# Performance work log

Measured on AMD Instinct MI355X. Metric: run time of the kernel, lower is better.

## Reference

```python
import jax, jax.numpy as jnp
import numpy as np

TOKENS = 8192
IN_FEATURES = 4096
OUT_FEATURES = 4096
ALPHA = 2e-05
BETA = 8.0


def setup_inputs() -> dict:
    key = jax.random.key(0)
    kx, kw = jax.random.split(key)
    # int8 activations and weights, values in [-127, 127]
    x = jax.random.randint(kx, (TOKENS, IN_FEATURES), -127, 128, dtype=jnp.int32).astype(jnp.int8)
    weight = jax.random.randint(kw, (OUT_FEATURES, IN_FEATURES), -127, 128, dtype=jnp.int32).astype(jnp.int8)
    bias = jnp.zeros((OUT_FEATURES,), dtype=jnp.float32)
    a = jnp.float32(ALPHA)  # dequant scale: input_scale * weight_scale
    b = jnp.float32(BETA)   # requant scale: 1 / out_scale
    return {"x": x, "weight": weight, "bias": bias, "a": a, "b": b}


def reference(x, weight, bias, a, b):
    acc = jnp.matmul(x.astype(jnp.int32), weight.T.astype(jnp.int32))
    # fp32 epilogue: dequant scale + bias, exact GeLU, requant by beta
    y = a * acc.astype(jnp.float32) + bias[None, :]
    y = jax.nn.gelu(y, approximate=False)
    # quantize output to int8 (round to nearest even, saturate)
    q = jnp.clip(jnp.rint(y * b), -128.0, 127.0).astype(jnp.int8)
    return q
```

## Files before the change

kernel.cpp:

```cpp
#include <hip/hip_runtime.h>
#include <cstdint>
#include <cstddef>

#define TOKENS 8192
#define INF    4096
#define OUTF   4096

typedef int v4i __attribute__((ext_vector_type(4)));

__global__ __launch_bounds__(256) void pack_i8_kernel(
    const int* __restrict__ xi, const int* __restrict__ wi,
    uint8_t* __restrict__ x8, uint8_t* __restrict__ w8) {
  const int NX = (TOKENS * INF) / 4;
  const int NT = 2048 * 256;
  int tid = blockIdx.x * 256 + threadIdx.x;
#pragma unroll 1
  for (int it = 0; it < 24; ++it) {
    int c = it * NT + tid;
    const int4* src;
    unsigned* dst;
    if (c < NX) {
      src = (const int4*)xi + c;
      dst = (unsigned*)x8 + c;
    } else {
      int c2 = c - NX;
      src = (const int4*)wi + c2;
      dst = (unsigned*)w8 + c2;
    }
    int4 v = *src;
    *dst = (v.x & 255) | ((v.y & 255) << 8) | ((v.z & 255) << 16) |
           (((unsigned)v.w) << 24);
  }
}

__device__ __forceinline__ float gelu_exact(float y) {
  float x = y * 0.70710678118654752f;
  float s = fabsf(x);
  float t = __builtin_amdgcn_rcpf(fmaf(s, 0.3275911f, 1.0f));
  float p = t * fmaf(t, fmaf(t, fmaf(t, fmaf(t, 1.061405429f, -1.453152027f),
                                     1.421413741f), -0.284496736f),
                     0.254829592f);
  float e = __expf(-s * s);
  float er = fmaf(-p, e, 1.0f);
  er = copysignf(er, x);
  return 0.5f * y * (1.0f + er);
}

__global__ __launch_bounds__(512, 2) void gemm_i8_gelu_q_kernel(
    const uint8_t* __restrict__ x8, const uint8_t* __restrict__ w8,
    const float* __restrict__ bias, const float* __restrict__ pa,
    const float* __restrict__ pb, int* __restrict__ out) {
  __shared__ char sm[65536];

  const int tid = threadIdx.x;
  const int l   = tid & 63;
  const int wv  = tid >> 6;
  const int wr  = wv >> 2;
  const int wc  = wv & 3;
  const int lr  = l & 15;
  const int lg  = l >> 4;

  int id = blockIdx.x;
  int wg = (id & 7) * 64 + (id >> 3);
  const int m0 = (wg >> 4) * 256;
  const int n0 = (wg & 15) * 256;

  const float av = pa[0];
  const float bv = pb[0];

  const int srow  = tid >> 3;
  const int sslot = tid & 7;
  const int wslot = ((sslot ^ (srow & 7)) << 4);
  const uint8_t* ga = x8 + (size_t)(m0 + srow) * INF + sslot * 16;
  const uint8_t* gb = w8 + (size_t)(n0 + srow) * INF + sslot * 16;
  const int lds_w = srow * 128 + wslot;

  int aoff[8], boff[4], sb[2];
#pragma unroll
  for (int m = 0; m < 8; ++m) aoff[m] = (wr * 128 + m * 16 + lr) * 128;
#pragma unroll
  for (int n = 0; n < 4; ++n) boff[n] = 32768 + (wc * 64 + n * 16 + lr) * 128;
#pragma unroll
  for (int s = 0; s < 2; ++s) sb[s] = (((s * 4 + lg) ^ (l & 7)) << 4);

  v4i acc[8][4];
#pragma unroll
  for (int m = 0; m < 8; ++m)
#pragma unroll
    for (int n = 0; n < 4; ++n) acc[m][n] = (v4i){0, 0, 0, 0};

  v4i avr[4], bvr[4];
#pragma unroll
  for (int i = 0; i < 4; ++i) {
    avr[i] = *(const v4i*)(ga + (size_t)i * 64 * INF);
    bvr[i] = *(const v4i*)(gb + (size_t)i * 64 * INF);
  }

  const int NKT = INF / 128;
#pragma unroll 1
  for (int kt = 0; kt < NKT; ++kt) {
    asm volatile("" ::: "memory");
    __builtin_amdgcn_s_barrier();
    asm volatile("" ::: "memory");
#pragma unroll
    for (int i = 0; i < 4; ++i) {
      *(v4i*)(sm + i * 8192 + lds_w)         = avr[i];
      *(v4i*)(sm + 32768 + i * 8192 + lds_w) = bvr[i];
    }
    __syncthreads();

    if (kt + 1 < NKT) {
      const uint8_t* ga2 = ga + (size_t)(kt + 1) * 128;
      const uint8_t* gb2 = gb + (size_t)(kt + 1) * 128;
#pragma unroll
      for (int i = 0; i < 4; ++i) {
        avr[i] = *(const v4i*)(ga2 + (size_t)i * 64 * INF);
        bvr[i] = *(const v4i*)(gb2 + (size_t)i * 64 * INF);
      }
    }

#pragma unroll
    for (int s = 0; s < 2; ++s) {
      v4i Af[8], Bf[4];
#pragma unroll
      for (int m = 0; m < 8; ++m) Af[m] = *(const v4i*)(sm + aoff[m] + sb[s]);
#pragma unroll
      for (int n = 0; n < 4; ++n) Bf[n] = *(const v4i*)(sm + boff[n] + sb[s]);
#pragma unroll
      for (int m = 0; m < 8; ++m)
#pragma unroll
        for (int n = 0; n < 4; ++n)
          acc[m][n] = __builtin_amdgcn_mfma_i32_16x16x64_i8(Af[m], Bf[n],
                                                            acc[m][n], 0, 0, 0);
    }
  }

  float bvals[4];
#pragma unroll
  for (int n = 0; n < 4; ++n) bvals[n] = bias[n0 + wc * 64 + n * 16 + lr];

#pragma unroll
  for (int m = 0; m < 8; ++m) {
    int rowb = m0 + wr * 128 + m * 16 + lg * 4;
#pragma unroll
    for (int q = 0; q < 4; ++q) {
      size_t rb = (size_t)(rowb + q) * OUTF;
#pragma unroll
      for (int n = 0; n < 4; ++n) {
        float f = fmaf(av, (float)acc[m][n][q], bvals[n]);
        float g = gelu_exact(f);
        float r = __builtin_rintf(g * bv);
        r = fminf(fmaxf(r, -128.0f), 127.0f);
        out[rb + (size_t)(n0 + wc * 64 + n * 16 + lr)] = (int)r;
      }
    }
  }
}

extern "C" void kernel_launch(void* const* d_in, const int* in_sizes, int n_in,
                              void* d_out, int out_size, void* d_ws,
                              size_t ws_size, hipStream_t stream) {
  const int*   xi   = (const int*)d_in[0];
  const int*   wi   = (const int*)d_in[1];
  const float* bias = (const float*)d_in[2];
  const float* pa   = (const float*)d_in[3];
  const float* pb   = (const float*)d_in[4];
  int*         out  = (int*)d_out;

  uint8_t* x8 = (uint8_t*)d_ws;
  uint8_t* w8 = x8 + (size_t)TOKENS * INF;

  pack_i8_kernel<<<2048, 256, 0, stream>>>(xi, wi, x8, w8);

  dim3 grid((TOKENS / 256) * (OUTF / 256));
  gemm_i8_gelu_q_kernel<<<grid, 512, 0, stream>>>(x8, w8, bias, pa, pb, out);
}
```

Baseline: 417.6 us.

## Use direct global-to-LDS loads with double-buffered LDS and phased MFMA scheduling

Replaces the register-staged global loads and LDS stores with global_load_lds direct-to-LDS transfers into a double-buffered 128KB shared memory region, prefetching two k-tiles ahead. The compute loop is split into four phases separated by barriers, with s_setprio raised around MFMA bursts so waves interleave LDS reads and matrix ops. The intent is to remove VGPR staging and LDS write instructions and to overlap memory traffic with compute. The cost is double the LDS use, which with 512 threads and a 2-block launch bound may limit occupancy to one block per CU, plus extra barriers per tile.

```diff
diff --git a/kernel.cpp b/kernel.cpp
--- a/kernel.cpp
+++ b/kernel.cpp
@@ -46,11 +46,17 @@
   return 0.5f * y * (1.0f + er);
 }
 
+__device__ __forceinline__ void barrier_fenced() {
+  asm volatile("" ::: "memory");
+  __builtin_amdgcn_s_barrier();
+  asm volatile("" ::: "memory");
+}
+
 __global__ __launch_bounds__(512, 2) void gemm_i8_gelu_q_kernel(
     const uint8_t* __restrict__ x8, const uint8_t* __restrict__ w8,
     const float* __restrict__ bias, const float* __restrict__ pa,
     const float* __restrict__ pb, int* __restrict__ out) {
-  __shared__ char sm[65536];
+  __shared__ char sm[131072];
 
   const int tid = threadIdx.x;
   const int l   = tid & 63;
@@ -68,12 +74,11 @@
   const float av = pa[0];
   const float bv = pb[0];
 
-  const int srow  = tid >> 3;
-  const int sslot = tid & 7;
-  const int wslot = ((sslot ^ (srow & 7)) << 4);
-  const uint8_t* ga = x8 + (size_t)(m0 + srow) * INF + sslot * 16;
-  const uint8_t* gb = w8 + (size_t)(n0 + srow) * INF + sslot * 16;
-  const int lds_w = srow * 128 + wslot;
+  const int grow = (wv << 5) + (l >> 3);
+  const int gch  = ((l & 7) ^ ((l >> 3) & 7)) << 4;
+  const uint8_t* gA = x8 + (size_t)(m0 + grow) * INF + gch;
+  const uint8_t* gB = w8 + (size_t)(n0 + grow) * INF + gch;
+  const int ldsw = (wv << 2) * 1024;
 
   int aoff[8], boff[4], sb[2];
 #pragma unroll
@@ -89,50 +94,76 @@
 #pragma unroll
     for (int n = 0; n < 4; ++n) acc[m][n] = (v4i){0, 0, 0, 0};
 
-  v4i avr[4], bvr[4];
-#pragma unroll
-  for (int i = 0; i < 4; ++i) {
-    avr[i] = *(const v4i*)(ga + (size_t)i * 64 * INF);
-    bvr[i] = *(const v4i*)(gb + (size_t)i * 64 * INF);
-  }
+#define BURST(kt, bo)                                                         \
+  {                                                                           \
+    _Pragma("unroll")                                                         \
+    for (int i = 0; i < 4; ++i) {                                             \
+      __builtin_amdgcn_global_load_lds(                                       \
+          (const __attribute__((address_space(1))) unsigned*)(                \
+              gA + (size_t)i * 8 * INF + (size_t)(kt) * 128),                 \
+          (__attribute__((address_space(3))) unsigned*)(sm + (bo) + ldsw +    \
+                                                        i * 1024),            \
+          16, 0, 0);                                                          \
+      __builtin_amdgcn_global_load_lds(                                       \
+          (const __attribute__((address_space(1))) unsigned*)(                \
+              gB + (size_t)i * 8 * INF + (size_t)(kt) * 128),                 \
+          (__attribute__((address_space(3))) unsigned*)(sm + (bo) + 32768 +   \
+                                                        ldsw + i * 1024),     \
+          16, 0, 0);                                                          \
+    }                                                                         \
+  }
+
+#define LDV4(off) (*(const v4i*)(sm + bo + (off)))
+
+#define PHASE(mb, ks, READB)                                                  \
+  {                                                                           \
+    if (READB) {                                                              \
+      _Pragma("unroll")                                                       \
+      for (int n = 0; n < 4; ++n) Bf[n] = LDV4(boff[n] + sb[ks]);             \
+    }                                                                         \
+    v4i A0 = LDV4(aoff[(mb) + 0] + sb[ks]);                                   \
+    v4i A1 = LDV4(aoff[(mb) + 1] + sb[ks]);                                   \
+    v4i A2 = LDV4(aoff[(mb) + 2] + sb[ks]);                                   \
+    v4i A3 = LDV4(aoff[(mb) + 3] + sb[ks]);                                   \
+    barrier_fenced();                                                         \
+    asm volatile("s_waitcnt lgkmcnt(0)" ::: "memory");                        \
+    __builtin_amdgcn_s_setprio(1);                                            \
+    _Pragma("unroll")                                                         \
+    for (int n = 0; n < 4; ++n) {                                             \
+      acc[(mb) + 0][n] = __builtin_amdgcn_mfma_i32_16x16x64_i8(               \
+          A0, Bf[n], acc[(mb) + 0][n], 0, 0, 0);                              \
+      acc[(mb) + 1][n] = __builtin_amdgcn_mfma_i32_16x16x64_i8(               \
+          A1, Bf[n], acc[(mb) + 1][n], 0, 0, 0);                              \
+      acc[(mb) + 2][n] = __builtin_amdgcn_mfma_i32_16x16x64_i8(               \
+          A2, Bf[n], acc[(mb) + 2][n], 0, 0, 0);                              \
+      acc[(mb) + 3][n] = __builtin_amdgcn_mfma_i32_16x16x64_i8(               \
+          A3, Bf[n], acc[(mb) + 3][n], 0, 0, 0);                              \
+    }                                                                         \
+    __builtin_amdgcn_s_setprio(0);                                            \
+    __builtin_amdgcn_s_barrier();                                             \
+    asm volatile("" ::: "memory");                                            \
+  }
+
+  BURST(0, 0);
+  BURST(1, 65536);
 
   const int NKT = INF / 128;
 #pragma unroll 1
   for (int kt = 0; kt < NKT; ++kt) {
-    asm volatile("" ::: "memory");
-    __builtin_amdgcn_s_barrier();
-    asm volatile("" ::: "memory");
-#pragma unroll
-    for (int i = 0; i < 4; ++i) {
-      *(v4i*)(sm + i * 8192 + lds_w)         = avr[i];
-      *(v4i*)(sm + 32768 + i * 8192 + lds_w) = bvr[i];
+    const int bo = (kt & 1) << 16;
+    if (kt < NKT - 1) {
+      asm volatile("s_waitcnt vmcnt(8)" ::: "memory");
+    } else {
+      asm volatile("s_waitcnt vmcnt(0)" ::: "memory");
     }
-    __syncthreads();
-
-    if (kt + 1 < NKT) {
-      const uint8_t* ga2 = ga + (size_t)(kt + 1) * 128;
-      const uint8_t* gb2 = gb + (size_t)(kt + 1) * 128;
-#pragma unroll
-      for (int i = 0; i < 4; ++i) {
-        avr[i] = *(const v4i*)(ga2 + (size_t)i * 64 * INF);
-        bvr[i] = *(const v4i*)(gb2 + (size_t)i * 64 * INF);
-      }
-    }
-
-#pragma unroll
-    for (int s = 0; s < 2; ++s) {
-      v4i Af[8], Bf[4];
-#pragma unroll
-      for (int m = 0; m < 8; ++m) Af[m] = *(const v4i*)(sm + aoff[m] + sb[s]);
-#pragma unroll
-      for (int n = 0; n < 4; ++n) Bf[n] = *(const v4i*)(sm + boff[n] + sb[s]);
-#pragma unroll
-      for (int m = 0; m < 8; ++m)
-#pragma unroll
-        for (int n = 0; n < 4; ++n)
-          acc[m][n] = __builtin_amdgcn_mfma_i32_16x16x64_i8(Af[m], Bf[n],
-                                                            acc[m][n], 0, 0, 0);
-    }
+    barrier_fenced();
+
+    v4i Bf[4];
+    PHASE(0, 0, 1)
+    PHASE(4, 0, 0)
+    PHASE(0, 1, 1)
+    PHASE(4, 1, 0)
+    if (kt + 2 < NKT) BURST(kt + 2, bo);
   }
 
   float bvals[4];
@@ -155,6 +186,9 @@
       }
     }
   }
+#undef BURST
+#undef LDV4
+#undef PHASE
 }
 
 extern "C" void kernel_launch(void* const* d_in, const int* in_sizes, int n_in,
```

After: 425.3 us. No clear change (+1.9%).

## Pipeline GEMM mainloop with direct global-to-LDS loads and 4-stage LDS ring

Applied to the files above, without the earlier changes.

Replaces the register-staged global load plus LDS store with global_load_lds direct copies into a 4-slot LDS ring of 64-byte K halves, issuing loads three stages ahead. The MFMA work is split into quarter blocks interleaved with partial fragment reads, barriers and setprio, to overlap memory and matrix math. The pack kernel also batches four independent loads per iteration to expose memory-level parallelism. LDS use doubles to 128 KB per block, which may limit occupancy to one block per CU, and the hand-counted vmcnt waits add correctness fragility.

```diff
diff --git a/kernel.cpp b/kernel.cpp
--- a/kernel.cpp
+++ b/kernel.cpp
@@ -15,21 +15,23 @@
   const int NT = 2048 * 256;
   int tid = blockIdx.x * 256 + threadIdx.x;
 #pragma unroll 1
-  for (int it = 0; it < 24; ++it) {
-    int c = it * NT + tid;
-    const int4* src;
-    unsigned* dst;
-    if (c < NX) {
-      src = (const int4*)xi + c;
-      dst = (unsigned*)x8 + c;
-    } else {
-      int c2 = c - NX;
-      src = (const int4*)wi + c2;
-      dst = (unsigned*)w8 + c2;
+  for (int g = 0; g < 6; ++g) {
+    int c[4];
+    int4 v[4];
+#pragma unroll
+    for (int j = 0; j < 4; ++j) {
+      c[j] = (g * 4 + j) * NT + tid;
+      const int4* src = (c[j] < NX) ? ((const int4*)xi + c[j])
+                                    : ((const int4*)wi + (c[j] - NX));
+      v[j] = *src;
     }
-    int4 v = *src;
-    *dst = (v.x & 255) | ((v.y & 255) << 8) | ((v.z & 255) << 16) |
-           (((unsigned)v.w) << 24);
+#pragma unroll
+    for (int j = 0; j < 4; ++j) {
+      unsigned* dst = (c[j] < NX) ? ((unsigned*)x8 + c[j])
+                                  : ((unsigned*)w8 + (c[j] - NX));
+      *dst = (v[j].x & 255) | ((v[j].y & 255) << 8) | ((v[j].z & 255) << 16) |
+             (((unsigned)v[j].w) << 24);
+    }
   }
 }
 
@@ -46,11 +48,17 @@
   return 0.5f * y * (1.0f + er);
 }
 
+__device__ __forceinline__ void barrier_fenced() {
+  asm volatile("" ::: "memory");
+  __builtin_amdgcn_s_barrier();
+  asm volatile("" ::: "memory");
+}
+
 __global__ __launch_bounds__(512, 2) void gemm_i8_gelu_q_kernel(
     const uint8_t* __restrict__ x8, const uint8_t* __restrict__ w8,
     const float* __restrict__ bias, const float* __restrict__ pa,
     const float* __restrict__ pb, int* __restrict__ out) {
-  __shared__ char sm[65536];
+  __shared__ char sm[131072];
 
   const int tid = threadIdx.x;
   const int l   = tid & 63;
@@ -68,20 +76,19 @@
   const float av = pa[0];
   const float bv = pb[0];
 
-  const int srow  = tid >> 3;
-  const int sslot = tid & 7;
-  const int wslot = ((sslot ^ (srow & 7)) << 4);
-  const uint8_t* ga = x8 + (size_t)(m0 + srow) * INF + sslot * 16;
-  const uint8_t* gb = w8 + (size_t)(n0 + srow) * INF + sslot * 16;
-  const int lds_w = srow * 128 + wslot;
-
-  int aoff[8], boff[4], sb[2];
-#pragma unroll
-  for (int m = 0; m < 8; ++m) aoff[m] = (wr * 128 + m * 16 + lr) * 128;
-#pragma unroll
-  for (int n = 0; n < 4; ++n) boff[n] = 32768 + (wc * 64 + n * 16 + lr) * 128;
-#pragma unroll
-  for (int s = 0; s < 2; ++s) sb[s] = (((s * 4 + lg) ^ (l & 7)) << 4);
+  const int srow4 = l >> 2;
+  const int schu  = ((l & 3) ^ (srow4 & 3)) << 4;
+  const uint8_t* bA = x8 + (size_t)(m0 + wv * 16 + srow4) * INF + schu;
+  const uint8_t* bB = w8 + (size_t)(n0 + wv * 16 + srow4) * INF + schu;
+  const int dA = wv * 1024;
+
+  int aoff[8], boff[4];
+#pragma unroll
+  for (int m = 0; m < 8; ++m)
+    aoff[m] = (wr * 128 + m * 16 + lr) * 64 + ((lg ^ (lr & 3)) << 4);
+#pragma unroll
+  for (int n = 0; n < 4; ++n)
+    boff[n] = 65536 + (wc * 64 + n * 16 + lr) * 64 + ((lg ^ (lr & 3)) << 4);
 
   v4i acc[8][4];
 #pragma unroll
@@ -89,51 +96,92 @@
 #pragma unroll
     for (int n = 0; n < 4; ++n) acc[m][n] = (v4i){0, 0, 0, 0};
 
-  v4i avr[4], bvr[4];
-#pragma unroll
-  for (int i = 0; i < 4; ++i) {
-    avr[i] = *(const v4i*)(ga + (size_t)i * 64 * INF);
-    bvr[i] = *(const v4i*)(gb + (size_t)i * 64 * INF);
-  }
-
-  const int NKT = INF / 128;
+#define GLL(gsrc, ldst)                                                       \
+  __builtin_amdgcn_global_load_lds(                                           \
+      (const __attribute__((address_space(1))) unsigned*)(gsrc),              \
+      (__attribute__((address_space(3))) unsigned*)(ldst), 16, 0, 0);
+
+#define GLA(H, J) GLL(bA + (size_t)(H) * 64 + (size_t)(J) * 128 * INF,        \
+                      sm + (((H) & 3) << 14) + (J) * 8192 + dA)
+#define GLB(H, J) GLL(bB + (size_t)(H) * 64 + (size_t)(J) * 128 * INF,        \
+                      sm + 65536 + (((H) & 3) << 14) + (J) * 8192 + dA)
+
+#define MM(m, n) acc[m][n] = __builtin_amdgcn_mfma_i32_16x16x64_i8(           \
+                     Af[m], Bf[n], acc[m][n], 0, 0, 0)
+
+#define PRE_MFMA                                                              \
+  barrier_fenced();                                                           \
+  asm volatile("s_waitcnt lgkmcnt(0)" ::: "memory");                          \
+  __builtin_amdgcn_s_setprio(1);
+#define POST_MFMA                                                             \
+  __builtin_amdgcn_s_setprio(0);                                              \
+  barrier_fenced();
+
+#define HALF(H, S, DOSTAGE, NW)                                               \
+  {                                                                           \
+    const char* sb_ = sm + ((S) << 14);                                       \
+    v4i Af[8], Bf[4];                                                         \
+                                        \
+    Af[0] = *(const v4i*)(sb_ + aoff[0]);                                     \
+    Af[1] = *(const v4i*)(sb_ + aoff[1]);                                     \
+    Af[2] = *(const v4i*)(sb_ + aoff[2]);                                     \
+    Af[3] = *(const v4i*)(sb_ + aoff[3]);                                     \
+    Bf[0] = *(const v4i*)(sb_ + boff[0]);                                     \
+    Bf[1] = *(const v4i*)(sb_ + boff[1]);                                     \
+    if (DOSTAGE) { GLA((H) + 3, 0); }                                         \
+    PRE_MFMA                                                                  \
+    MM(0, 0); MM(0, 1); MM(1, 0); MM(1, 1);                                   \
+    MM(2, 0); MM(2, 1); MM(3, 0); MM(3, 1);                                   \
+    POST_MFMA                                                                 \
+                                             \
+    Af[4] = *(const v4i*)(sb_ + aoff[4]);                                     \
+    Af[5] = *(const v4i*)(sb_ + aoff[5]);                                     \
+    Af[6] = *(const v4i*)(sb_ + aoff[6]);                                     \
+    Af[7] = *(const v4i*)(sb_ + aoff[7]);                                     \
+    if (DOSTAGE) { GLA((H) + 3, 1); }                                         \
+    PRE_MFMA                                                                  \
+    MM(4, 0); MM(4, 1); MM(5, 0); MM(5, 1);                                   \
+    MM(6, 0); MM(6, 1); MM(7, 0); MM(7, 1);                                   \
+    POST_MFMA                                                                 \
+                                             \
+    Bf[2] = *(const v4i*)(sb_ + boff[2]);                                     \
+    Bf[3] = *(const v4i*)(sb_ + boff[3]);                                     \
+    if (DOSTAGE) { GLB((H) + 3, 0); }                                         \
+    PRE_MFMA                                                                  \
+    MM(0, 2); MM(0, 3); MM(1, 2); MM(1, 3);                                   \
+    MM(2, 2); MM(2, 3); MM(3, 2); MM(3, 3);                                   \
+    POST_MFMA                                                                 \
+           \
+    if (DOSTAGE) { GLB((H) + 3, 1); }                                         \
+    barrier_fenced();                                                         \
+    __builtin_amdgcn_s_setprio(1);                                            \
+    MM(4, 2); MM(4, 3); MM(5, 2); MM(5, 3);                                   \
+    MM(6, 2); MM(6, 3); MM(7, 2); MM(7, 3);                                   \
+    __builtin_amdgcn_s_setprio(0);                                            \
+    if ((NW) == 8) { asm volatile("s_waitcnt vmcnt(8)" ::: "memory"); }       \
+    else if ((NW) == 4) { asm volatile("s_waitcnt vmcnt(4)" ::: "memory"); }  \
+    else if ((NW) == 0) { asm volatile("s_waitcnt vmcnt(0)" ::: "memory"); }  \
+    if ((NW) >= 0) { barrier_fenced(); }                                      \
+  }
+
+#pragma unroll
+  for (int hh = 0; hh < 3; ++hh) {
+    GLA(hh, 0); GLA(hh, 1); GLB(hh, 0); GLB(hh, 1);
+  }
+  asm volatile("s_waitcnt vmcnt(8)" ::: "memory");
+  barrier_fenced();
+
 #pragma unroll 1
-  for (int kt = 0; kt < NKT; ++kt) {
-    asm volatile("" ::: "memory");
-    __builtin_amdgcn_s_barrier();
-    asm volatile("" ::: "memory");
-#pragma unroll
-    for (int i = 0; i < 4; ++i) {
-      *(v4i*)(sm + i * 8192 + lds_w)         = avr[i];
-      *(v4i*)(sm + 32768 + i * 8192 + lds_w) = bvr[i];
-    }
-    __syncthreads();
-
-    if (kt + 1 < NKT) {
-      const uint8_t* ga2 = ga + (size_t)(kt + 1) * 128;
-      const uint8_t* gb2 = gb + (size_t)(kt + 1) * 128;
-#pragma unroll
-      for (int i = 0; i < 4; ++i) {
-        avr[i] = *(const v4i*)(ga2 + (size_t)i * 64 * INF);
-        bvr[i] = *(const v4i*)(gb2 + (size_t)i * 64 * INF);
-      }
-    }
-
-#pragma unroll
-    for (int s = 0; s < 2; ++s) {
-      v4i Af[8], Bf[4];
-#pragma unroll
-      for (int m = 0; m < 8; ++m) Af[m] = *(const v4i*)(sm + aoff[m] + sb[s]);
-#pragma unroll
-      for (int n = 0; n < 4; ++n) Bf[n] = *(const v4i*)(sm + boff[n] + sb[s]);
-#pragma unroll
-      for (int m = 0; m < 8; ++m)
-#pragma unroll
-        for (int n = 0; n < 4; ++n)
-          acc[m][n] = __builtin_amdgcn_mfma_i32_16x16x64_i8(Af[m], Bf[n],
-                                                            acc[m][n], 0, 0, 0);
-    }
-  }
+  for (int hb = 0; hb < 60; hb += 4) {
+    HALF(hb + 0, 0, 1, 8)
+    HALF(hb + 1, 1, 1, 8)
+    HALF(hb + 2, 2, 1, 8)
+    HALF(hb + 3, 3, 1, 8)
+  }
+  HALF(60, 0, 1, 8)
+  HALF(61, 1, 0, 4)
+  HALF(62, 2, 0, 0)
+  HALF(63, 3, 0, -1)
 
   float bvals[4];
 #pragma unroll
@@ -155,6 +203,13 @@
       }
     }
   }
+#undef GLL
+#undef GLA
+#undef GLB
+#undef MM
+#undef PRE_MFMA
+#undef POST_MFMA
+#undef HALF
 }
 
 extern "C" void kernel_launch(void* const* d_in, const int* in_sizes, int n_in,
```

Measured after the change: 411.9 us. About the same (-1.4%).
